# Kernel optimization log

Hardware: AMD Instinct MI355X
Metric: run time of the kernel (lower is better)

## Reference

```python
import jax, jax.numpy as jnp
import numpy as np

EPS = 1e-15  # matches torch_geometric GMMConv


def setup_inputs() -> dict:
    key = jax.random.key(0)
    ks = jax.random.split(key, 8)
    N, E, C_in, C_out, K, D = 163842, 1146894, 32, 32, 6, 3
    x = jax.random.normal(ks[0], (N, C_in), dtype=jnp.float32)
    edge_index = jax.random.randint(ks[1], (2, E), 0, N, dtype=jnp.int64)
    pseudo = jax.random.uniform(ks[2], (E, D), dtype=jnp.float32)
    g = jax.random.normal(ks[3], (C_in, K * C_out), dtype=jnp.float32) / np.sqrt(C_in)
    mu = jax.random.normal(ks[4], (K, D), dtype=jnp.float32)
    sigma = jax.random.uniform(ks[5], (K, D), dtype=jnp.float32) + 0.5
    root = jax.random.normal(ks[6], (C_in, C_out), dtype=jnp.float32) / np.sqrt(C_in)
    bias = jnp.zeros((C_out,), dtype=jnp.float32)
    return {"x": x, "edge_index": edge_index, "pseudo": pseudo, "g": g,
            "mu": mu, "sigma": sigma, "root": root, "bias": bias}


def reference(x, edge_index, pseudo, g, mu, sigma, root, bias):
    N = x.shape[0]
    K, D = mu.shape
    C_out = g.shape[1] // K
    src, dst = edge_index[0], edge_index[1]
    # per-node transform then gather per edge: [N, K, C_out] -> [E, K, C_out]
    xg = (x @ g).reshape(N, K, C_out)
    # Gaussian mixture weights on edge pseudo-coordinates: [E, K]
    diff = pseudo[:, None, :] - mu[None, :, :]              # [E, K, D]
    gauss = jnp.exp(jnp.sum(-0.5 * diff * diff / (EPS + sigma * sigma)[None], axis=-1))
    # weighted sum over kernels -> per-edge message [E, C_out]
    msg = jnp.einsum('eko,ek->eo', xg[src], gauss)
    # mean aggregation at destination nodes
    agg = jax.ops.segment_sum(msg, dst, num_segments=N)
    cnt = jax.ops.segment_sum(jnp.ones((src.shape[0],), x.dtype), dst, num_segments=N)
    out = agg / jnp.maximum(cnt, 1.0)[:, None]
    # root weight and bias (PyG defaults root_weight=True, bias=True)
    return out + x @ root + bias
```

## Files before the change

kernel.cpp:

```cpp
#include <hip/hip_runtime.h>
#include <hip/hip_bf16.h>

#define KD 6
#define DD 3
#define CO 32
#define CI 32
#define KC (KD * CO)
#define QP (KC / 2)

__global__ void xg_kernel(const float* __restrict__ x, const float* __restrict__ g,
                          uint* __restrict__ xg, int N) {
    __shared__ float gs[CI * KC];
    for (int i = threadIdx.x; i < CI * KC; i += blockDim.x) gs[i] = g[i];
    __syncthreads();
    const int total = N * QP;
    for (int idx = blockIdx.x * blockDim.x + threadIdx.x; idx < total;
         idx += gridDim.x * blockDim.x) {
        const int n = idx / QP;
        const int q = idx - n * QP;
        const float* xr = x + n * CI;
        const float* gq = gs + 2 * q;
        float a0 = 0.f, a1 = 0.f;
#pragma unroll
        for (int c = 0; c < CI; ++c) {
            float xc = xr[c];
            a0 = fmaf(xc, gq[c * KC], a0);
            a1 = fmaf(xc, gq[c * KC + 1], a1);
        }
        uint lo = (uint)__bfloat16_as_ushort(__float2bfloat16(a0));
        uint hi = (uint)__bfloat16_as_ushort(__float2bfloat16(a1));
        xg[idx] = lo | (hi << 16);
    }
}

__global__ void edge_kernel(const int* __restrict__ ei, const float* __restrict__ pseudo,
                            const ushort* __restrict__ xg, const float* __restrict__ mu,
                            const float* __restrict__ sigma,
                            float* __restrict__ agg, float* __restrict__ cnt, int E) {
    float m[KD][DD], iv[KD][DD];
#pragma unroll
    for (int k = 0; k < KD; ++k)
#pragma unroll
        for (int d = 0; d < DD; ++d) {
            m[k][d] = mu[k * DD + d];
            float s = sigma[k * DD + d];
            iv[k][d] = -0.5f / (1e-15f + s * s);
        }
    const int o = threadIdx.x & 31;
    const int gpb = blockDim.x >> 5;
    int e0 = blockIdx.x * gpb + (threadIdx.x >> 5);
    const int estride = gridDim.x * gpb;
    for (int e = e0; e < E; e += estride) {
        const int src = ei[e];
        const int dst = ei[E + e];
        const float p0 = pseudo[e * 3 + 0];
        const float p1 = pseudo[e * 3 + 1];
        const float p2 = pseudo[e * 3 + 2];
        const ushort* xr = xg + (size_t)src * KC;
        float msg = 0.f;
#pragma unroll
        for (int k = 0; k < KD; ++k) {
            float d0 = p0 - m[k][0], d1 = p1 - m[k][1], d2 = p2 - m[k][2];
            float ex = d0 * d0 * iv[k][0] + d1 * d1 * iv[k][1] + d2 * d2 * iv[k][2];
            float w = __expf(ex);
            float xv = __uint_as_float(((uint)xr[k * CO + o]) << 16);
            msg = fmaf(w, xv, msg);
        }
        atomicAdd(&agg[(size_t)dst * CO + o], msg);
        if (o == 0) atomicAdd(&cnt[dst], 1.0f);
    }
}

__global__ void out_kernel(const float* __restrict__ x, const float* __restrict__ root,
                           const float* __restrict__ bias, const float* __restrict__ cnt,
                           float* __restrict__ out, int N) {
    __shared__ float rs[CI * CO];
    __shared__ float bs[CO];
    for (int i = threadIdx.x; i < CI * CO; i += blockDim.x) rs[i] = root[i];
    if (threadIdx.x < CO) bs[threadIdx.x] = bias[threadIdx.x];
    __syncthreads();
    int total = N * CO;
    for (int idx = blockIdx.x * blockDim.x + threadIdx.x; idx < total;
         idx += gridDim.x * blockDim.x) {
        int n = idx / CO;
        int o = idx - n * CO;
        const float* xr = x + n * CI;
        float acc = 0.f;
#pragma unroll
        for (int c = 0; c < CI; ++c) acc = fmaf(xr[c], rs[c * CO + o], acc);
        float cn = cnt[n];
        out[idx] = out[idx] / fmaxf(cn, 1.0f) + acc + bs[o];
    }
}

extern "C" void kernel_launch(void* const* d_in, const int* in_sizes, int n_in,
                              void* d_out, int out_size, void* d_ws, size_t ws_size,
                              hipStream_t stream) {
    const float* x      = (const float*)d_in[0];
    const int*   ei     = (const int*)d_in[1];
    const float* pseudo = (const float*)d_in[2];
    const float* g      = (const float*)d_in[3];
    const float* mu     = (const float*)d_in[4];
    const float* sigma  = (const float*)d_in[5];
    const float* root   = (const float*)d_in[6];
    const float* bias   = (const float*)d_in[7];
    float* out = (float*)d_out;

    const int N = in_sizes[0] / CI;
    const int E = in_sizes[1] / 2;

    ushort* xg = (ushort*)d_ws;
    float* cnt = (float*)(xg + (size_t)N * KC);

    hipMemsetAsync(d_out, 0, (size_t)out_size * sizeof(float), stream);
    hipMemsetAsync(cnt, 0, (size_t)N * sizeof(float), stream);

    const int blk = 256;

    int grid1 = (N * QP + blk - 1) / blk;
    if (grid1 > 4096) grid1 = 4096;
    xg_kernel<<<grid1, blk, 0, stream>>>(x, g, (uint*)xg, N);

    const int gpb = blk / 32;
    int grid2 = (E + gpb - 1) / gpb;
    if (grid2 > 16384) grid2 = 16384;
    edge_kernel<<<grid2, blk, 0, stream>>>(ei, pseudo, xg, mu, sigma, out, cnt, E);

    int grid3 = (N * CO + blk - 1) / blk;
    if (grid3 > 4096) grid3 = 4096;
    out_kernel<<<grid3, blk, 0, stream>>>(x, root, bias, cnt, out, N);
}
```

Measured before the change: 373.0 us.

## Precompute per-edge Gaussian weights, register-tile xg GEMM, vectorize edge and output kernels

Adds a separate kernel that computes the six Gaussian mixture weights per edge once and stores them packed as bf16 in a 16-byte record. This removes the redundant exp computation that each of the 32 lanes did per edge. The xg kernel now computes 4 nodes by 4 outputs per thread with float4 shared-memory reads. The edge kernel reads packed bf16 pairs as uint, splits the kernels across half-warps and combines the halves with a shuffle. The output kernel handles 4 channels per thread with float4 loads and stores. The cost is an extra pass that writes and reads E×16 bytes of weights, plus an extra kernel launch.

```diff
diff --git a/kernel.cpp b/kernel.cpp
--- a/kernel.cpp
+++ b/kernel.cpp
@@ -8,35 +8,16 @@
 #define KC (KD * CO)
 #define QP (KC / 2)
 
-__global__ void xg_kernel(const float* __restrict__ x, const float* __restrict__ g,
-                          uint* __restrict__ xg, int N) {
-    __shared__ float gs[CI * KC];
-    for (int i = threadIdx.x; i < CI * KC; i += blockDim.x) gs[i] = g[i];
-    __syncthreads();
-    const int total = N * QP;
-    for (int idx = blockIdx.x * blockDim.x + threadIdx.x; idx < total;
-         idx += gridDim.x * blockDim.x) {
-        const int n = idx / QP;
-        const int q = idx - n * QP;
-        const float* xr = x + n * CI;
-        const float* gq = gs + 2 * q;
-        float a0 = 0.f, a1 = 0.f;
-#pragma unroll
-        for (int c = 0; c < CI; ++c) {
-            float xc = xr[c];
-            a0 = fmaf(xc, gq[c * KC], a0);
-            a1 = fmaf(xc, gq[c * KC + 1], a1);
-        }
-        uint lo = (uint)__bfloat16_as_ushort(__float2bfloat16(a0));
-        uint hi = (uint)__bfloat16_as_ushort(__float2bfloat16(a1));
-        xg[idx] = lo | (hi << 16);
-    }
+__device__ __forceinline__ uint pack_bf16(float a, float b) {
+    uint lo = (uint)__bfloat16_as_ushort(__float2bfloat16(a));
+    uint hi = (uint)__bfloat16_as_ushort(__float2bfloat16(b));
+    return lo | (hi << 16);
 }
+__device__ __forceinline__ float bf_lo(uint u) { return __uint_as_float(u << 16); }
+__device__ __forceinline__ float bf_hi(uint u) { return __uint_as_float(u & 0xffff0000u); }
 
-__global__ void edge_kernel(const int* __restrict__ ei, const float* __restrict__ pseudo,
-                            const ushort* __restrict__ xg, const float* __restrict__ mu,
-                            const float* __restrict__ sigma,
-                            float* __restrict__ agg, float* __restrict__ cnt, int E) {
+__global__ void gauss_kernel(const float* __restrict__ pseudo, const float* __restrict__ mu,
+                             const float* __restrict__ sigma, uint4* __restrict__ W, int E) {
     float m[KD][DD], iv[KD][DD];
 #pragma unroll
     for (int k = 0; k < KD; ++k)
@@ -46,28 +27,96 @@
             float s = sigma[k * DD + d];
             iv[k][d] = -0.5f / (1e-15f + s * s);
         }
-    const int o = threadIdx.x & 31;
+    for (int e = blockIdx.x * blockDim.x + threadIdx.x; e < E;
+         e += gridDim.x * blockDim.x) {
+        float p0 = pseudo[3 * e], p1 = pseudo[3 * e + 1], p2 = pseudo[3 * e + 2];
+        float w[KD];
+#pragma unroll
+        for (int k = 0; k < KD; ++k) {
+            float d0 = p0 - m[k][0], d1 = p1 - m[k][1], d2 = p2 - m[k][2];
+            w[k] = __expf(d0 * d0 * iv[k][0] + d1 * d1 * iv[k][1] + d2 * d2 * iv[k][2]);
+        }
+        W[e] = make_uint4(pack_bf16(w[0], w[1]), pack_bf16(w[2], w[3]),
+                          pack_bf16(w[4], w[5]), 0u);
+    }
+}
+
+__global__ void xg_kernel(const float* __restrict__ x, const float* __restrict__ g,
+                          uint* __restrict__ xg, int N) {
+    __shared__ float gs[CI * KC];
+    for (int i = threadIdx.x; i < CI * KC; i += blockDim.x) gs[i] = g[i];
+    __syncthreads();
+    const int NB = (N + 3) >> 2;
+    const int total = NB * 48;
+    for (int idx = blockIdx.x * blockDim.x + threadIdx.x; idx < total;
+         idx += gridDim.x * blockDim.x) {
+        const int b = idx / 48;
+        const int t = idx - b * 48;
+        const int n0 = b * 4;
+        const float* xr[4];
+#pragma unroll
+        for (int r = 0; r < 4; ++r) {
+            int n = n0 + r; if (n > N - 1) n = N - 1;
+            xr[r] = x + (size_t)n * CI;
+        }
+        float acc[4][4];
+#pragma unroll
+        for (int r = 0; r < 4; ++r)
+#pragma unroll
+            for (int j = 0; j < 4; ++j) acc[r][j] = 0.f;
+#pragma unroll
+        for (int c = 0; c < CI; ++c) {
+            const float4 gv = *(const float4*)&gs[c * KC + 4 * t];
+#pragma unroll
+            for (int r = 0; r < 4; ++r) {
+                float xc = xr[r][c];
+                acc[r][0] = fmaf(xc, gv.x, acc[r][0]);
+                acc[r][1] = fmaf(xc, gv.y, acc[r][1]);
+                acc[r][2] = fmaf(xc, gv.z, acc[r][2]);
+                acc[r][3] = fmaf(xc, gv.w, acc[r][3]);
+            }
+        }
+#pragma unroll
+        for (int r = 0; r < 4; ++r) {
+            int n = n0 + r;
+            if (n < N) {
+                uint2 pk = make_uint2(pack_bf16(acc[r][0], acc[r][1]),
+                                      pack_bf16(acc[r][2], acc[r][3]));
+                *(uint2*)(xg + (size_t)n * QP + 2 * t) = pk;
+            }
+        }
+    }
+}
+
+__global__ void edge_kernel(const int* __restrict__ ei, const uint4* __restrict__ W,
+                            const uint* __restrict__ xg,
+                            float* __restrict__ agg, float* __restrict__ cnt, int E) {
+    const int l = threadIdx.x & 31;
+    const int kbase = l >> 4;
+    const int p = l & 15;
     const int gpb = blockDim.x >> 5;
-    int e0 = blockIdx.x * gpb + (threadIdx.x >> 5);
+    const int e0 = blockIdx.x * gpb + (threadIdx.x >> 5);
     const int estride = gridDim.x * gpb;
     for (int e = e0; e < E; e += estride) {
         const int src = ei[e];
         const int dst = ei[E + e];
-        const float p0 = pseudo[e * 3 + 0];
-        const float p1 = pseudo[e * 3 + 1];
-        const float p2 = pseudo[e * 3 + 2];
-        const ushort* xr = xg + (size_t)src * KC;
-        float msg = 0.f;
-#pragma unroll
-        for (int k = 0; k < KD; ++k) {
-            float d0 = p0 - m[k][0], d1 = p1 - m[k][1], d2 = p2 - m[k][2];
-            float ex = d0 * d0 * iv[k][0] + d1 * d1 * iv[k][1] + d2 * d2 * iv[k][2];
-            float w = __expf(ex);
-            float xv = __uint_as_float(((uint)xr[k * CO + o]) << 16);
-            msg = fmaf(w, xv, msg);
-        }
-        atomicAdd(&agg[(size_t)dst * CO + o], msg);
-        if (o == 0) atomicAdd(&cnt[dst], 1.0f);
+        const uint4 wv = W[e];
+        float wa = __uint_as_float((kbase ? (wv.x >> 16) : (wv.x & 0xffffu)) << 16);
+        float wb = __uint_as_float((kbase ? (wv.y >> 16) : (wv.y & 0xffffu)) << 16);
+        float wc = __uint_as_float((kbase ? (wv.z >> 16) : (wv.z & 0xffffu)) << 16);
+        const uint* xr = xg + (size_t)src * QP;
+        const uint u0 = xr[l];
+        const uint u1 = xr[l + 32];
+        const uint u2 = xr[l + 64];
+        float s0 = wa * bf_lo(u0), s1 = wa * bf_hi(u0);
+        s0 = fmaf(wb, bf_lo(u1), s0); s1 = fmaf(wb, bf_hi(u1), s1);
+        s0 = fmaf(wc, bf_lo(u2), s0); s1 = fmaf(wc, bf_hi(u2), s1);
+        s0 += __shfl_xor(s0, 16);
+        s1 += __shfl_xor(s1, 16);
+        const float val = kbase ? s1 : s0;
+        const int ch = 2 * p + kbase;
+        atomicAdd(&agg[(size_t)dst * CO + ch], val);
+        if (l == 0) atomicAdd(&cnt[dst], 1.0f);
     }
 }
 
@@ -79,17 +128,30 @@
     for (int i = threadIdx.x; i < CI * CO; i += blockDim.x) rs[i] = root[i];
     if (threadIdx.x < CO) bs[threadIdx.x] = bias[threadIdx.x];
     __syncthreads();
-    int total = N * CO;
+    const int total = N * 8;
     for (int idx = blockIdx.x * blockDim.x + threadIdx.x; idx < total;
          idx += gridDim.x * blockDim.x) {
-        int n = idx / CO;
-        int o = idx - n * CO;
-        const float* xr = x + n * CI;
-        float acc = 0.f;
+        const int n = idx >> 3;
+        const int t = idx & 7;
+        const float* xr = x + (size_t)n * CI;
+        float a0 = 0.f, a1 = 0.f, a2 = 0.f, a3 = 0.f;
 #pragma unroll
-        for (int c = 0; c < CI; ++c) acc = fmaf(xr[c], rs[c * CO + o], acc);
-        float cn = cnt[n];
-        out[idx] = out[idx] / fmaxf(cn, 1.0f) + acc + bs[o];
+        for (int c = 0; c < CI; ++c) {
+            const float4 rv = *(const float4*)&rs[c * CO + 4 * t];
+            float xc = xr[c];
+            a0 = fmaf(xc, rv.x, a0);
+            a1 = fmaf(xc, rv.y, a1);
+            a2 = fmaf(xc, rv.z, a2);
+            a3 = fmaf(xc, rv.w, a3);
+        }
+        const float inv = 1.0f / fmaxf(cnt[n], 1.0f);
+        float4 o = *(float4*)&out[(size_t)n * CO + 4 * t];
+        const float4 bv = *(const float4*)&bs[4 * t];
+        o.x = o.x * inv + a0 + bv.x;
+        o.y = o.y * inv + a1 + bv.y;
+        o.z = o.z * inv + a2 + bv.z;
+        o.w = o.w * inv + a3 + bv.w;
+        *(float4*)&out[(size_t)n * CO + 4 * t] = o;
     }
 }
 
@@ -109,24 +171,25 @@
     const int N = in_sizes[0] / CI;
     const int E = in_sizes[1] / 2;
 
-    ushort* xg = (ushort*)d_ws;
-    float* cnt = (float*)(xg + (size_t)N * KC);
+    uint*  xg = (uint*)d_ws;
+    uint4* W  = (uint4*)(xg + (size_t)N * QP);
+    float* cnt = (float*)(W + E);
 
     hipMemsetAsync(d_out, 0, (size_t)out_size * sizeof(float), stream);
     hipMemsetAsync(cnt, 0, (size_t)N * sizeof(float), stream);
 
     const int blk = 256;
 
-    int grid1 = (N * QP + blk - 1) / blk;
-    if (grid1 > 4096) grid1 = 4096;
-    xg_kernel<<<grid1, blk, 0, stream>>>(x, g, (uint*)xg, N);
+    gauss_kernel<<<(E + blk - 1) / blk, blk, 0, stream>>>(pseudo, mu, sigma, W, E);
+
+    xg_kernel<<<2048, blk, 0, stream>>>(x, g, xg, N);
 
     const int gpb = blk / 32;
     int grid2 = (E + gpb - 1) / gpb;
     if (grid2 > 16384) grid2 = 16384;
-    edge_kernel<<<grid2, blk, 0, stream>>>(ei, pseudo, xg, mu, sigma, out, cnt, E);
+    edge_kernel<<<grid2, blk, 0, stream>>>(ei, W, xg, out, cnt, E);
 
-    int grid3 = (N * CO + blk - 1) / blk;
+    int grid3 = (N * 8 + blk - 1) / blk;
     if (grid3 > 4096) grid3 = 4096;
     out_kernel<<<grid3, blk, 0, stream>>>(x, root, bias, cnt, out, N);
 }
```

Result: slower. 959.3 us (+157.2%).
